# Kernel optimization log

Hardware: AMD Instinct MI355X
Metric: run time of the kernel (lower is better)

The kernel has to match this reference:

```python
import jax, jax.numpy as jnp
import numpy as np

NUM_HEADS = 16

def setup_inputs() -> dict:
    key = jax.random.key(0)
    k_x, k_wq, k_bq, k_wo, k_bo = jax.random.split(key, 5)
    B, S, D = 4, 2048, 1024
    x = jax.random.normal(k_x, (B, S, D), dtype=jnp.float32)
    # Flax Dense default init: lecun_normal for kernel, zeros for bias; use small normals here.
    w_qkv = jax.random.normal(k_wq, (D, 3 * D), dtype=jnp.float32) * (D ** -0.5)
    b_qkv = jnp.zeros((3 * D,), dtype=jnp.float32)
    w_out = jax.random.normal(k_wo, (D, D), dtype=jnp.float32) * (D ** -0.5)
    b_out = jnp.zeros((D,), dtype=jnp.float32)
    return {"x": x, "w_qkv": w_qkv, "b_qkv": b_qkv, "w_out": w_out, "b_out": b_out}

def reference(x, w_qkv, b_qkv, w_out, b_out):
    B, S, D = x.shape
    H = NUM_HEADS
    hd = D // H
    scale = hd ** -0.5
    qkv = x @ w_qkv + b_qkv                                  # [B,S,3D]
    qkv = qkv.reshape(B, S, 3, H, hd)
    qkv = jnp.transpose(qkv, (2, 0, 3, 1, 4))                # [3,B,H,S,hd]
    q, k, v = qkv[0], qkv[1], qkv[2]
    attn = jnp.einsum("bhqd,bhkd->bhqk", q, k) * scale       # [B,H,S,S]
    attn = jax.nn.softmax(attn, axis=-1)
    out = jnp.einsum("bhqk,bhkd->bhqd", attn, v)             # [B,H,S,hd]
    out = jnp.transpose(out, (0, 2, 1, 3)).reshape(B, S, D)
    return out @ w_out + b_out
```

## Files before the change

### kernel.cpp

```cpp
#include <hip/hip_runtime.h>
#include <cstdint>
#include <cstddef>

#define B_    4
#define S_    2048
#define D_    1024
#define H_    16
#define HD_   64
#define M_    8192
#define NQKV  3072

typedef __bf16 bf16;
typedef __bf16 bf16x4 __attribute__((ext_vector_type(4)));
typedef __bf16 bf16x8 __attribute__((ext_vector_type(8)));
typedef float  f32x4  __attribute__((ext_vector_type(4)));
typedef float  f32x16 __attribute__((ext_vector_type(16)));
typedef unsigned short u16x4 __attribute__((ext_vector_type(4)));
typedef uint32_t u32x4 __attribute__((ext_vector_type(4)));

__device__ __forceinline__ void gl2lds16(const void* g, void* l) {
  __builtin_amdgcn_global_load_lds(
      (__attribute__((address_space(1))) void*)(uintptr_t)g,
      (__attribute__((address_space(3))) void*)l, 16, 0, 0);
}

__device__ __forceinline__ uint32_t pkbf16(float a, float b) {
  union { bf16 h[2]; uint32_t u; } z;
  z.h[0] = (bf16)a; z.h[1] = (bf16)b;
  return z.u;
}

__global__ __launch_bounds__(256) void cast_f32_bf16(const float* __restrict__ in,
                                                     bf16* __restrict__ out, int n4) {
  int i = blockIdx.x * 256 + threadIdx.x;
  if (i >= n4) return;
  float4 v = ((const float4*)in)[i];
  bf16x4 o;
  o[0] = (bf16)v.x; o[1] = (bf16)v.y; o[2] = (bf16)v.z; o[3] = (bf16)v.w;
  ((bf16x4*)out)[i] = o;
}

__global__ __launch_bounds__(256) void transpose_cast(const float* __restrict__ in,
                                                      bf16* __restrict__ out, int R, int C) {
  __shared__ float tile[32][33];
  int bx = blockIdx.x * 32, by = blockIdx.y * 32;
  int tx = threadIdx.x, ty = threadIdx.y;
#pragma unroll
  for (int i = 0; i < 32; i += 8)
    tile[ty + i][tx] = in[(size_t)(by + ty + i) * C + bx + tx];
  __syncthreads();
#pragma unroll
  for (int i = 0; i < 32; i += 8)
    out[(size_t)(bx + ty + i) * R + by + tx] = (bf16)tile[tx][ty + i];
}

template <bool OUT_BF16>
__global__ __launch_bounds__(256) void gemm_bt(const bf16* __restrict__ A,
                                               const bf16* __restrict__ Bt,
                                               const float* __restrict__ bias,
                                               void* __restrict__ Cptr,
                                               int M, int N, int K) {
  __shared__ __align__(16) bf16 As[128 * 64];
  __shared__ __align__(16) bf16 Bs[128 * 64];
  const int tid  = threadIdx.x;
  const int lane = tid & 63, w = tid >> 6;
  const int lo   = lane & 15, quad = lane >> 4;
  const int bm = blockIdx.y * 128, bn = blockIdx.x * 128;
  const int wm = (w >> 1) * 64,    wn = (w & 1) * 64;

  f32x4 acc[4][4];
  const f32x4 zero = {0.f, 0.f, 0.f, 0.f};
#pragma unroll
  for (int i = 0; i < 4; ++i)
#pragma unroll
    for (int j = 0; j < 4; ++j) acc[i][j] = zero;

  for (int k0 = 0; k0 < K; k0 += 64) {
#pragma unroll
    for (int c = 0; c < 4; ++c) {
      int seg = c * 4 + w;
      int idx = seg * 512 + lane * 8;
      int row = idx >> 6, col = idx & 63;
      gl2lds16(A  + (size_t)(bm + row) * K + k0 + col, As + seg * 512);
      gl2lds16(Bt + (size_t)(bn + row) * K + k0 + col, Bs + seg * 512);
    }
    __syncthreads();
#pragma unroll
    for (int ks = 0; ks < 2; ++ks) {
      bf16x8 av[4], bv[4];
#pragma unroll
      for (int i = 0; i < 4; ++i)
        av[i] = *(const bf16x8*)&As[(wm + i * 16 + lo) * 64 + ks * 32 + quad * 8];
#pragma unroll
      for (int j = 0; j < 4; ++j)
        bv[j] = *(const bf16x8*)&Bs[(wn + j * 16 + lo) * 64 + ks * 32 + quad * 8];
#pragma unroll
      for (int i = 0; i < 4; ++i)
#pragma unroll
        for (int j = 0; j < 4; ++j)
          acc[i][j] = __builtin_amdgcn_mfma_f32_16x16x32_bf16(av[i], bv[j], acc[i][j], 0, 0, 0);
    }
    __syncthreads();
  }
#pragma unroll
  for (int j = 0; j < 4; ++j) {
    int cg = bn + wn + j * 16 + lo;
    float bsv = bias[cg];
#pragma unroll
    for (int i = 0; i < 4; ++i) {
      int rg = bm + wm + i * 16 + quad * 4;
#pragma unroll
      for (int r = 0; r < 4; ++r) {
        float v = acc[i][j][r] + bsv;
        if (OUT_BF16) ((bf16*)Cptr)[(size_t)(rg + r) * N + cg] = (bf16)v;
        else          ((float*)Cptr)[(size_t)(rg + r) * N + cg] = v;
      }
    }
  }
}

#define PSTR 72

__global__ __launch_bounds__(256, 3) void flash_attn(const bf16* __restrict__ qkv,
                                                     bf16* __restrict__ out) {
  __shared__ __align__(16) bf16 Ks[2][64 * PSTR];
  __shared__ __align__(16) bf16 Vs[2][64 * PSTR];

  const int tid  = threadIdx.x;
  const int lane = tid & 63, wq = tid >> 6;
  const int l31  = lane & 31;
  const int e    = lane >> 5;
  const int hi8  = e * 8, hi4 = e * 4;

  const int bid = blockIdx.x;
  const int qb  = bid >> 6;
  const int bh  = bid & 63;
  const int h   = bh & 15;
  const int b   = bh >> 4;
  const int q0  = qb * 128;
  const size_t rowb = (size_t)b * S_;
  const bf16* qbase = qkv + rowb * NQKV + h * HD_;
  const bf16* kbase = qbase + D_;
  const bf16* vbase = qbase + 2 * D_;

  bf16x8 qf[4];
  {
    const bf16* qrow = qbase + (size_t)(q0 + wq * 32 + l31) * NQKV;
#pragma unroll
    for (int c = 0; c < 4; ++c)
      qf[c] = *(const bf16x8*)(qrow + c * 16 + hi8);
  }

  int ks_s[2], ks_d[2];
#pragma unroll
  for (int c = 0; c < 2; ++c) {
    int idx = c * 256 + tid;
    ks_s[c] = idx >> 3;
    ks_d[c] = (idx & 7) * 8;
  }
  int vs_d[2], vs_s[2];
#pragma unroll
  for (int u = 0; u < 2; ++u) {
    int idx = u * 256 + tid;
    vs_d[u] = (idx & 31) * 2;
    vs_s[u] = (idx >> 5) * 4;
  }

  uint4 kreg[2];
  uint32_t vreg[2][4];

#pragma unroll
  for (int c = 0; c < 2; ++c)
    kreg[c] = *(const uint4*)(kbase + (size_t)ks_s[c] * NQKV + ks_d[c]);
#pragma unroll
  for (int u = 0; u < 2; ++u)
#pragma unroll
    for (int j = 0; j < 4; ++j)
      vreg[u][j] = *(const uint32_t*)(vbase + (size_t)(vs_s[u] + j) * NQKV + vs_d[u]);

  const f32x16 zero16 = {0.f,0.f,0.f,0.f,0.f,0.f,0.f,0.f,0.f,0.f,0.f,0.f,0.f,0.f,0.f,0.f};
  f32x16 oacc[2];
  oacc[0] = zero16; oacc[1] = zero16;
  float lsum = 0.f;
  const float c2 = 0.125f * 1.44269504088896341f;

  for (int kt = 0; kt < 32; ++kt) {
    const int buf = kt & 1;
#pragma unroll
    for (int c = 0; c < 2; ++c)
      *(uint4*)&Ks[buf][ks_s[c] * PSTR + ks_d[c]] = kreg[c];
#pragma unroll
    for (int u = 0; u < 2; ++u) {
      int d0 = vs_d[u], s0 = vs_s[u];
      u16x4 lo, hi;
#pragma unroll
      for (int j = 0; j < 4; ++j) {
        lo[j] = (unsigned short)(vreg[u][j] & 0xffffu);
        hi[j] = (unsigned short)(vreg[u][j] >> 16);
      }
      *(u16x4*)&Vs[buf][(d0 + 0) * PSTR + s0] = lo;
      *(u16x4*)&Vs[buf][(d0 + 1) * PSTR + s0] = hi;
    }
    __syncthreads();

    {
      int ktn = (kt + 1 < 32) ? kt + 1 : 31;
      const bf16* kb = kbase + (size_t)ktn * 64 * NQKV;
      const bf16* vb = vbase + (size_t)ktn * 64 * NQKV;
#pragma unroll
      for (int c = 0; c < 2; ++c)
        kreg[c] = *(const uint4*)(kb + (size_t)ks_s[c] * NQKV + ks_d[c]);
#pragma unroll
      for (int u = 0; u < 2; ++u)
#pragma unroll
        for (int j = 0; j < 4; ++j)
          vreg[u][j] = *(const uint32_t*)(vb + (size_t)(vs_s[u] + j) * NQKV + vs_d[u]);
    }

    f32x16 sacc[2];
#pragma unroll
    for (int kk = 0; kk < 2; ++kk) {
      sacc[kk] = zero16;
      int srow = kk * 32 + l31;
#pragma unroll
      for (int c = 0; c < 4; ++c) {
        bf16x8 kf = *(const bf16x8*)&Ks[buf][srow * PSTR + c * 16 + hi8];
        sacc[kk] = __builtin_amdgcn_mfma_f32_32x32x16_bf16(kf, qf[c], sacc[kk], 0, 0, 0);
      }
    }

#pragma unroll
    for (int kk = 0; kk < 2; ++kk) {
      uint32_t Q8[8];
      float ps = 0.f;
#pragma unroll
      for (int i = 0; i < 8; ++i) {
        float p0 = __builtin_amdgcn_exp2f(sacc[kk][2 * i]     * c2 - 16.0f);
        float p1 = __builtin_amdgcn_exp2f(sacc[kk][2 * i + 1] * c2 - 16.0f);
        ps += p0 + p1;
        Q8[i] = pkbf16(p0, p1);
      }
      lsum += ps;
#pragma unroll
      for (int mh = 0; mh < 2; ++mh) {
        const int m = kk * 2 + mh, bq = mh * 4;
        uint32_t s0 = e ? Q8[bq]     : Q8[bq + 2];
        uint32_t s1 = e ? Q8[bq + 1] : Q8[bq + 3];
        uint32_t r0 = __shfl_xor(s0, 32);
        uint32_t r1 = __shfl_xor(s1, 32);
        u32x4 pd;
        pd[0] = e ? r0 : Q8[bq];
        pd[1] = e ? r1 : Q8[bq + 1];
        pd[2] = e ? Q8[bq + 2] : r0;
        pd[3] = e ? Q8[bq + 3] : r1;
        bf16x8 pf = __builtin_bit_cast(bf16x8, pd);
#pragma unroll
        for (int dt = 0; dt < 2; ++dt) {
          int drow = dt * 32 + l31;
          bf16x8 vf = *(const bf16x8*)&Vs[buf][drow * PSTR + m * 16 + hi8];
          oacc[dt] = __builtin_amdgcn_mfma_f32_32x32x16_bf16(vf, pf, oacc[dt], 0, 0, 0);
        }
      }
    }
  }

  lsum += __shfl_xor(lsum, 32);

  __syncthreads();
  bf16* Os = (bf16*)Ks;
  {
    float inv = 1.f / lsum;
    int ql = wq * 32 + l31;
#pragma unroll
    for (int dt = 0; dt < 2; ++dt) {
#pragma unroll
      for (int g = 0; g < 4; ++g) {
        bf16x4 ov;
#pragma unroll
        for (int jj = 0; jj < 4; ++jj) ov[jj] = (bf16)(oacc[dt][g * 4 + jj] * inv);
        *(bf16x4*)&Os[ql * PSTR + dt * 32 + g * 8 + hi4] = ov;
      }
    }
  }
  __syncthreads();
#pragma unroll
  for (int it = 0; it < 4; ++it) {
    int idx = it * 256 + tid;
    int row = idx >> 3, c8 = (idx & 7) * 8;
    bf16x8 t = *(const bf16x8*)&Os[row * PSTR + c8];
    *(bf16x8*)&out[(rowb + q0 + row) * D_ + h * HD_ + c8] = t;
  }
}

extern "C" void kernel_launch(void* const* d_in, const int* in_sizes, int n_in,
                              void* d_out, int out_size, void* d_ws, size_t ws_size,
                              hipStream_t stream) {
  const float* x     = (const float*)d_in[0];
  const float* w_qkv = (const float*)d_in[1];
  const float* b_qkv = (const float*)d_in[2];
  const float* w_out = (const float*)d_in[3];
  const float* b_out = (const float*)d_in[4];
  float* out = (float*)d_out;

  char* ws = (char*)d_ws;
  bf16* xb    = (bf16*)(ws);
  bf16* wqkvT = (bf16*)(ws + (size_t)16777216);
  bf16* woutT = (bf16*)(ws + (size_t)23068672);
  bf16* qkvb  = (bf16*)(ws + (size_t)25165824);
  bf16* attnb = (bf16*)(ws + (size_t)75497472);

  cast_f32_bf16<<<(M_ * D_ / 4 + 255) / 256, 256, 0, stream>>>(x, xb, M_ * D_ / 4);
  transpose_cast<<<dim3(NQKV / 32, D_ / 32), dim3(32, 8), 0, stream>>>(w_qkv, wqkvT, D_, NQKV);
  transpose_cast<<<dim3(D_ / 32, D_ / 32), dim3(32, 8), 0, stream>>>(w_out, woutT, D_, D_);

  gemm_bt<true><<<dim3(NQKV / 128, M_ / 128), 256, 0, stream>>>(
      xb, wqkvT, b_qkv, (void*)qkvb, M_, NQKV, D_);

  flash_attn<<<B_ * H_ * (S_ / 128), 256, 0, stream>>>(qkvb, attnb);

  gemm_bt<false><<<dim3(D_ / 128, M_ / 128), 256, 0, stream>>>(
      attnb, woutT, b_out, (void*)out, M_, D_, D_);
}
```

Baseline: 331.4 us.

## Load K tiles directly to LDS with XOR swizzle and remap GEMM blocks per XCD

In the attention kernel, K tiles are now fetched with global_load_lds into an unpadded, XOR-swizzled LDS buffer. This replaces the register staging and explicit LDS stores, frees registers, and raises the launch-bounds occupancy hint from 3 to 4 blocks. The output staging buffer moves from Ks to Vs. The GEMMs switch to a 1D grid whose block index is decoded so consecutive blocks on the same XCD share M rows, aiming for better L2 reuse. The risks are hazards from the direct LDS loads and the mapping only covering grids whose shape fits the decoding.

New measurement: 306.3 us. -7.6%, faster.

```diff
diff --git a/kernel.cpp b/kernel.cpp
--- a/kernel.cpp
+++ b/kernel.cpp
@@ -65,7 +65,9 @@
   const int tid  = threadIdx.x;
   const int lane = tid & 63, w = tid >> 6;
   const int lo   = lane & 15, quad = lane >> 4;
-  const int bm = blockIdx.y * 128, bn = blockIdx.x * 128;
+  const int xcd = blockIdx.x & 7, g = blockIdx.x >> 3;
+  const int mi  = g & 7,          n = g >> 3;
+  const int bm  = (xcd * 8 + mi) * 128, bn = n * 128;
   const int wm = (w >> 1) * 64,    wn = (w & 1) * 64;
 
   f32x4 acc[4][4];
@@ -121,9 +123,9 @@
 
 #define PSTR 72
 
-__global__ __launch_bounds__(256, 3) void flash_attn(const bf16* __restrict__ qkv,
+__global__ __launch_bounds__(256, 4) void flash_attn(const bf16* __restrict__ qkv,
                                                      bf16* __restrict__ out) {
-  __shared__ __align__(16) bf16 Ks[2][64 * PSTR];
+  __shared__ __align__(16) bf16 Ks[2][64 * 64];
   __shared__ __align__(16) bf16 Vs[2][64 * PSTR];
 
   const int tid  = threadIdx.x;
@@ -151,12 +153,13 @@
       qf[c] = *(const bf16x8*)(qrow + c * 16 + hi8);
   }
 
-  int ks_s[2], ks_d[2];
-#pragma unroll
-  for (int c = 0; c < 2; ++c) {
-    int idx = c * 256 + tid;
-    ks_s[c] = idx >> 3;
-    ks_d[c] = (idx & 7) * 8;
+  int kq_off[2];
+#pragma unroll
+  for (int it = 0; it < 2; ++it) {
+    int ci = it * 256 + tid;
+    int s  = ci >> 3;
+    int x  = (ci & 7) ^ (s & 7);
+    kq_off[it] = s * NQKV + x * 8;
   }
   int vs_d[2], vs_s[2];
 #pragma unroll
@@ -166,12 +169,11 @@
     vs_s[u] = (idx >> 5) * 4;
   }
 
-  uint4 kreg[2];
   uint32_t vreg[2][4];
 
 #pragma unroll
-  for (int c = 0; c < 2; ++c)
-    kreg[c] = *(const uint4*)(kbase + (size_t)ks_s[c] * NQKV + ks_d[c]);
+  for (int it = 0; it < 2; ++it)
+    gl2lds16(kbase + kq_off[it], &Ks[0][(it * 256 + wq * 64) * 8]);
 #pragma unroll
   for (int u = 0; u < 2; ++u)
 #pragma unroll
@@ -187,9 +189,6 @@
   for (int kt = 0; kt < 32; ++kt) {
     const int buf = kt & 1;
 #pragma unroll
-    for (int c = 0; c < 2; ++c)
-      *(uint4*)&Ks[buf][ks_s[c] * PSTR + ks_d[c]] = kreg[c];
-#pragma unroll
     for (int u = 0; u < 2; ++u) {
       int d0 = vs_d[u], s0 = vs_s[u];
       u16x4 lo, hi;
@@ -206,10 +205,13 @@
     {
       int ktn = (kt + 1 < 32) ? kt + 1 : 31;
       const bf16* kb = kbase + (size_t)ktn * 64 * NQKV;
+#pragma unroll
+      for (int it = 0; it < 2; ++it)
+        gl2lds16(kb + kq_off[it], &Ks[buf ^ 1][(it * 256 + wq * 64) * 8]);
+    }
+    {
+      int ktn = (kt + 1 < 32) ? kt + 1 : 31;
       const bf16* vb = vbase + (size_t)ktn * 64 * NQKV;
-#pragma unroll
-      for (int c = 0; c < 2; ++c)
-        kreg[c] = *(const uint4*)(kb + (size_t)ks_s[c] * NQKV + ks_d[c]);
 #pragma unroll
       for (int u = 0; u < 2; ++u)
 #pragma unroll
@@ -222,9 +224,10 @@
     for (int kk = 0; kk < 2; ++kk) {
       sacc[kk] = zero16;
       int srow = kk * 32 + l31;
+      int swz  = (srow & 7) * 8;
 #pragma unroll
       for (int c = 0; c < 4; ++c) {
-        bf16x8 kf = *(const bf16x8*)&Ks[buf][srow * PSTR + c * 16 + hi8];
+        bf16x8 kf = *(const bf16x8*)&Ks[buf][srow * 64 + ((c * 16 + hi8) ^ swz)];
         sacc[kk] = __builtin_amdgcn_mfma_f32_32x32x16_bf16(kf, qf[c], sacc[kk], 0, 0, 0);
       }
     }
@@ -267,7 +270,7 @@
   lsum += __shfl_xor(lsum, 32);
 
   __syncthreads();
-  bf16* Os = (bf16*)Ks;
+  bf16* Os = (bf16*)Vs;
   {
     float inv = 1.f / lsum;
     int ql = wq * 32 + l31;
@@ -313,11 +316,11 @@
   transpose_cast<<<dim3(NQKV / 32, D_ / 32), dim3(32, 8), 0, stream>>>(w_qkv, wqkvT, D_, NQKV);
   transpose_cast<<<dim3(D_ / 32, D_ / 32), dim3(32, 8), 0, stream>>>(w_out, woutT, D_, D_);
 
-  gemm_bt<true><<<dim3(NQKV / 128, M_ / 128), 256, 0, stream>>>(
+  gemm_bt<true><<<(M_ / 128) * (NQKV / 128), 256, 0, stream>>>(
       xb, wqkvT, b_qkv, (void*)qkvb, M_, NQKV, D_);
 
   flash_attn<<<B_ * H_ * (S_ / 128), 256, 0, stream>>>(qkvb, attnb);
 
-  gemm_bt<false><<<dim3(D_ / 128, M_ / 128), 256, 0, stream>>>(
+  gemm_bt<false><<<(M_ / 128) * (D_ / 128), 256, 0, stream>>>(
       attnb, woutT, b_out, (void*)out, M_, D_, D_);
 }
```
